# Performance work log

Measured on AMD Instinct MI355X. Metric: run time of the kernel, lower is better.

Reference implementation:

```python
import jax, jax.numpy as jnp
import numpy as np
from jax import lax


def setup_inputs() -> dict:
    key = jax.random.key(0)
    k1, k2 = jax.random.split(key)
    B, T, C, U, W = 8, 4096, 512, 512, 2
    inputs = jax.random.normal(k1, (B, T, C), dtype=jnp.float32)
    kernel = jax.random.normal(k2, (W, C, 3 * U), dtype=jnp.float32) * (1.0 / np.sqrt(W * C))
    bias = jnp.zeros((3 * U,), dtype=jnp.float32)
    return {"inputs": inputs, "kernel": kernel, "bias": bias}


def _fo_pool(x, f):
    # x, f: [B, T, U]; c_t = f_t * c_{t-1} + (1 - f_t) * x_t, c_0 = 0
    xT = jnp.swapaxes(x, 0, 1)  # [T, B, U]
    fT = jnp.swapaxes(f, 0, 1)
    c0 = jnp.zeros(x.shape[:1] + x.shape[2:], dtype=x.dtype)  # [B, U]

    def step(c, fx):
        ft, xt = fx
        c = ft * c + (1.0 - ft) * xt
        return c, c

    _, cT = lax.scan(step, c0, (fT, xT))
    return jnp.swapaxes(cT, 0, 1)  # [B, T, U]


def reference(inputs, kernel, bias):
    # Conv1D, padding='same', stride=1, NWC layout
    gates = lax.conv_general_dilated(
        inputs, kernel, window_strides=(1,), padding='SAME',
        dimension_numbers=('NWC', 'WIO', 'NWC')) + bias  # [B, T, 3U]
    x, forget, output = jnp.split(gates, 3, axis=-1)
    x = jnp.tanh(x)
    forget = jax.nn.sigmoid(forget)
    c = _fo_pool(x, forget)
    h = jax.nn.sigmoid(output) * c
    return h
```

## Files before the change

kernel.cpp:

```cpp
#include <hip/hip_runtime.h>

typedef unsigned short u16;
typedef unsigned int u32;
typedef _Float16 f16;
typedef __attribute__((ext_vector_type(8))) _Float16 half8;
typedef __attribute__((ext_vector_type(2))) __fp16 fp16x2;
typedef __attribute__((ext_vector_type(4))) float float4_;
typedef __attribute__((ext_vector_type(4))) unsigned short ushort4_;
typedef __attribute__((ext_vector_type(4))) unsigned int u32x4;

union hu { f16 h; u16 u; };

__device__ __forceinline__ u32 pkrtz(float a, float b) {
    fp16x2 t = __builtin_amdgcn_cvt_pkrtz(a, b);
    union { fp16x2 h; u32 u; } cv; cv.h = t;
    return cv.u;
}

__device__ __forceinline__ void gl16(const u16* g, u16* l) {
    __builtin_amdgcn_global_load_lds(
        (const __attribute__((address_space(1))) void*)g,
        (__attribute__((address_space(3))) void*)l, 16, 0, 0);
}

#define Bsz 8
#define Tsz 4096
#define Csz 512
#define Usz 512
#define NG  1536
#define KK  1024
#define MM  32768
#define NCH 128
#define CHL 32

__global__ void prep_a(const float* __restrict__ in, u16* __restrict__ A16) {
    int gid = blockIdx.x * 256 + threadIdx.x;
    int idx8 = gid * 8;
    int c8 = idx8 & 511;
    int row = idx8 >> 9;
    int b = (u32)row / 4097u;
    int t = row - b * 4097;
    u32x4 w;
    if (t == Tsz) {
        w = (u32x4)0;
    } else {
        const float* p = in + ((size_t)(b * Tsz + t) << 9) + c8;
        float4_ v0 = *(const float4_*)p;
        float4_ v1 = *(const float4_*)(p + 4);
        w.x = pkrtz(v0.x, v0.y); w.y = pkrtz(v0.z, v0.w);
        w.z = pkrtz(v1.x, v1.y); w.w = pkrtz(v1.z, v1.w);
    }
    *(u32x4*)(A16 + idx8) = w;
}

__global__ void prep_k(const float* __restrict__ kern, u16* __restrict__ KT) {
    __shared__ u16 t[64][70];
    const int k0 = blockIdx.x * 64;
    const int n0 = blockIdx.y * 64;
    const int tid = threadIdx.x;
    #pragma unroll
    for (int it = 0; it < 16; ++it) {
        int s = it * 256 + tid;
        int r = s >> 6;
        int c = s & 63;
        float v = kern[(size_t)(k0 + r) * NG + n0 + c];
        hu cv; cv.h = (f16)v;
        t[c][r] = cv.u;
    }
    __syncthreads();
    #pragma unroll
    for (int it = 0; it < 4; ++it) {
        int s = it * 256 + tid;
        int n = s >> 4;
        int kq = (s & 15) * 4;
        ushort4_ w;
        w.x = t[n][kq]; w.y = t[n][kq + 1]; w.z = t[n][kq + 2]; w.w = t[n][kq + 3];
        *(ushort4_*)(KT + (size_t)(n0 + n) * KK + k0 + kq) = w;
    }
}

#define LDS_A 8192
#define LDS_B 16384

__device__ __forceinline__ void stage_A(const u16* __restrict__ A16, u16* dst,
                                        int arow_base, int kin, int tid, int lane) {
    #pragma unroll
    for (int it = 0; it < 2; ++it) {
        int s = it * 512 + tid;
        int row = s >> 3, p = s & 7;
        int c = p ^ (row & 7);
        gl16(A16 + (((size_t)(arow_base + row)) << 9) + kin + c * 8, dst + (s - lane) * 8);
    }
}

__device__ __forceinline__ void stage_B_it(const u16* __restrict__ KT, u16* dst,
                                           int n0, int kc, int it, int tid, int lane) {
    int s = it * 512 + tid;
    int row = s >> 3, p = s & 7;
    int c = p ^ (row & 7);
    gl16(KT + (((size_t)(n0 + row)) << 10) + kc + c * 8, dst + (s - lane) * 8);
}

__global__ __launch_bounds__(512, 2) void gemm_gates(
    const u16* __restrict__ A16, const u16* __restrict__ KT,
    const float* __restrict__ bias,
    u16* __restrict__ X, u16* __restrict__ F, float* __restrict__ O)
{
    __shared__ u16 lA[3 * LDS_A];
    __shared__ u16 lB[3 * LDS_B];

    const int tid  = threadIdx.x;
    const int lane = tid & 63;
    const int wave = tid >> 6;

    const int orig = blockIdx.x;
    const int wg = (orig & 7) * 192 + (orig >> 3);
    const int nb = wg % 6;
    const int mb = wg / 6;
    const int m0 = mb * 128;
    const int n0 = nb * 256;
    const int b  = m0 >> 12;
    const int t0 = m0 & 4095;
    const int arow0 = b * (Tsz + 1) + t0;

    float4_ acc[4][4];
    #pragma unroll
    for (int i = 0; i < 4; ++i)
        #pragma unroll
        for (int j = 0; j < 4; ++j) acc[i][j] = (float4_)0.0f;

    const int wm = (wave >> 2) * 64;
    const int wn = (wave & 3) * 64;
    const int arow = wm + (lane & 15);
    const int brow = wn + (lane & 15);
    const int q   = lane >> 4;
    const int swz = lane & 7;

    stage_A(A16, lA, arow0, 0, tid, lane);
    #pragma unroll
    for (int it = 0; it < 4; ++it) stage_B_it(KT, lB, n0, 0, it, tid, lane);
    stage_A(A16, lA + LDS_A, arow0, 64, tid, lane);
    #pragma unroll
    for (int it = 0; it < 4; ++it) stage_B_it(KT, lB + LDS_B, n0, 64, it, tid, lane);

    int buf = 0;
    #pragma unroll 1
    for (int kt = 0; kt < 16; ++kt) {
        if (kt < 15) asm volatile("s_waitcnt vmcnt(6)" ::: "memory");
        else         asm volatile("s_waitcnt vmcnt(0)" ::: "memory");
        __builtin_amdgcn_s_barrier();

        const u16* a  = lA + buf * LDS_A;
        const u16* bs = lB + buf * LDS_B;
        const int nbuf = (buf >= 1) ? buf - 1 : 2;
        const int kt2 = kt + 2;
        const bool st = kt2 < 16;
        const int kc2 = kt2 * 64;

        half8 fa[4][2], fb01[2][2];
        #pragma unroll
        for (int mi = 0; mi < 4; ++mi)
            #pragma unroll
            for (int s2 = 0; s2 < 2; ++s2)
                fa[mi][s2] = *(const half8*)(a + (arow + mi * 16) * 64 + (((s2 * 4 + q) ^ swz) * 8));
        #pragma unroll
        for (int ni = 0; ni < 2; ++ni)
            #pragma unroll
            for (int s2 = 0; s2 < 2; ++s2)
                fb01[ni][s2] = *(const half8*)(bs + (brow + ni * 16) * 64 + (((s2 * 4 + q) ^ swz) * 8));
        if (st) {
            stage_A(A16, lA + nbuf * LDS_A, arow0 + (kt2 >> 3), (kt2 & 7) * 64, tid, lane);
            stage_B_it(KT, lB + nbuf * LDS_B, n0, kc2, 0, tid, lane);
        }
        __builtin_amdgcn_s_barrier();
        asm volatile("s_waitcnt lgkmcnt(0)" ::: "memory");
        __builtin_amdgcn_s_setprio(1);
        #pragma unroll
        for (int s2 = 0; s2 < 2; ++s2)
            #pragma unroll
            for (int mi = 0; mi < 4; ++mi)
                #pragma unroll
                for (int ni = 0; ni < 2; ++ni)
                    acc[mi][ni] = __builtin_amdgcn_mfma_f32_16x16x32_f16(fa[mi][s2], fb01[ni][s2], acc[mi][ni], 0, 0, 0);
        __builtin_amdgcn_s_setprio(0);
        __builtin_amdgcn_s_barrier();

        half8 fb23[2][2];
        #pragma unroll
        for (int ni = 0; ni < 2; ++ni)
            #pragma unroll
            for (int s2 = 0; s2 < 2; ++s2)
                fb23[ni][s2] = *(const half8*)(bs + (brow + 32 + ni * 16) * 64 + (((s2 * 4 + q) ^ swz) * 8));
        if (st) {
            stage_B_it(KT, lB + nbuf * LDS_B, n0, kc2, 1, tid, lane);
            stage_B_it(KT, lB + nbuf * LDS_B, n0, kc2, 2, tid, lane);
            stage_B_it(KT, lB + nbuf * LDS_B, n0, kc2, 3, tid, lane);
        }
        __builtin_amdgcn_s_barrier();
        asm volatile("s_waitcnt lgkmcnt(0)" ::: "memory");
        __builtin_amdgcn_s_setprio(1);
        #pragma unroll
        for (int s2 = 0; s2 < 2; ++s2)
            #pragma unroll
            for (int mi = 0; mi < 4; ++mi)
                #pragma unroll
                for (int ni = 0; ni < 2; ++ni)
                    acc[mi][ni + 2] = __builtin_amdgcn_mfma_f32_16x16x32_f16(fa[mi][s2], fb23[ni][s2], acc[mi][ni + 2], 0, 0, 0);
        __builtin_amdgcn_s_setprio(0);

        buf = (buf == 2) ? 0 : buf + 1;
    }

    const int plane = nb >> 1;
    const int rq = q * 4;
    const int cl = lane & 15;
    #pragma unroll
    for (int mi = 0; mi < 4; ++mi)
        #pragma unroll
        for (int ni = 0; ni < 4; ++ni) {
            const int gm = m0 + wm + mi * 16 + rq;
            const int gn = n0 + wn + ni * 16 + cl;
            const float bv = bias[gn];
            const int cp = gn & 511;
            #pragma unroll
            for (int r2 = 0; r2 < 4; ++r2) {
                float v = acc[mi][ni][r2] + bv;
                if (plane == 0) {
                    float res = 1.0f - 2.0f / (__expf(2.0f * v) + 1.0f);
                    hu cv; cv.h = (f16)res;
                    X[(size_t)(gm + r2) * Usz + cp] = cv.u;
                } else if (plane == 1) {
                    float res = 1.0f / (1.0f + __expf(-v));
                    hu cv; cv.h = (f16)res;
                    F[(size_t)(gm + r2) * Usz + cp] = cv.u;
                } else {
                    float res = 1.0f / (1.0f + __expf(-v));
                    O[(size_t)(gm + r2) * Usz + cp] = res;
                }
            }
        }
}

__device__ __forceinline__ float4_ x4(const u16* p) {
    ushort4_ xr = *(const ushort4_*)p;
    float4_ xv;
    #pragma unroll
    for (int j = 0; j < 4; ++j) { hu cv; cv.u = xr[j]; xv[j] = (float)cv.h; }
    return xv;
}

__global__ void scan_chunk(const u16* __restrict__ F, const u16* __restrict__ X,
                           float* __restrict__ CA, float* __restrict__ CB) {
    int g = blockIdx.x * 256 + threadIdx.x;
    int u4 = (g & 127) * 4;
    int bc = g >> 7;
    size_t base = (size_t)bc * CHL * Usz + u4;
    float4_ c = (float4_)0.0f, A = (float4_)1.0f;
    for (int i = 0; i < CHL; ++i) {
        float4_ fv = x4(F + base + (size_t)i * Usz);
        float4_ xv = x4(X + base + (size_t)i * Usz);
        c = fv * c + (1.0f - fv) * xv;
        A = A * fv;
    }
    *(float4_*)(CA + (size_t)bc * Usz + u4) = A;
    *(float4_*)(CB + (size_t)bc * Usz + u4) = c;
}

__global__ void scan_prefix(const float* __restrict__ CA, const float* __restrict__ CB,
                            float* __restrict__ CS) {
    int g = blockIdx.x * 256 + threadIdx.x;
    int u = g & 511;
    int b = g >> 9;
    float c = 0.0f;
    #pragma unroll 16
    for (int ch = 0; ch < NCH; ++ch) {
        int idx = (b * NCH + ch) * Usz + u;
        CS[idx] = c;
        c = CA[idx] * c + CB[idx];
    }
}

__global__ void scan_final(const u16* __restrict__ F, const u16* __restrict__ X,
                           const float* __restrict__ CS, float* __restrict__ out) {
    int g = blockIdx.x * 256 + threadIdx.x;
    int u4 = (g & 127) * 4;
    int bc = g >> 7;
    size_t base = (size_t)bc * CHL * Usz + u4;
    float4_ c = *(const float4_*)(CS + (size_t)bc * Usz + u4);
    for (int i = 0; i < CHL; ++i) {
        float4_ fv = x4(F + base + (size_t)i * Usz);
        float4_ xv = x4(X + base + (size_t)i * Usz);
        c = fv * c + (1.0f - fv) * xv;
        float4_ ov = *(const float4_*)(out + base + (size_t)i * Usz);
        *(float4_*)(out + base + (size_t)i * Usz) = ov * c;
    }
}

extern "C" void kernel_launch(void* const* d_in, const int* in_sizes, int n_in,
                              void* d_out, int out_size, void* d_ws, size_t ws_size,
                              hipStream_t stream) {
    const float* in   = (const float*)d_in[0];
    const float* kern = (const float*)d_in[1];
    const float* bias = (const float*)d_in[2];
    float* out = (float*)d_out;
    char* ws = (char*)d_ws;

    const size_t A16_B  = (size_t)Bsz * (Tsz + 1) * Csz * 2;
    const size_t OFF_KT = A16_B;
    const size_t OFF_F  = OFF_KT + (size_t)NG * KK * 2;
    const size_t OFF_X  = OFF_F + (size_t)MM * Usz * 2;
    const size_t NEED   = OFF_X + (size_t)MM * Usz * 2;

    if (ws_size < NEED) return;

    u16*   A16 = (u16*)ws;
    u16*   KT  = (u16*)(ws + OFF_KT);
    u16*   Fh  = (u16*)(ws + OFF_F);
    u16*   Xb  = (u16*)(ws + OFF_X);
    const size_t CH = (size_t)Bsz * NCH * Usz;
    float* CA = (float*)ws;
    float* CB = CA + CH;
    float* CS = CB + CH;

    prep_a<<<(int)(A16_B / 16 / 256), 256, 0, stream>>>(in, A16);
    prep_k<<<dim3(KK / 64, NG / 64), 256, 0, stream>>>(kern, KT);
    gemm_gates<<<(MM / 128) * (NG / 256), 512, 0, stream>>>(A16, KT, bias, Xb, Fh, out);
    scan_chunk<<<Bsz * NCH * Usz / 4 / 256, 256, 0, stream>>>(Fh, Xb, CA, CB);
    scan_prefix<<<Bsz * Usz / 256, 256, 0, stream>>>(CA, CB, CS);
    scan_final<<<Bsz * NCH * Usz / 4 / 256, 256, 0, stream>>>(Fh, Xb, CS, out);
}
```

Measured before the change: 317.0 us.

## Enlarge GEMM tile to 256x256 with K=32 stages and fewer barriers

The gates GEMM moves from a 128x256 block tile with 64-wide K stages to a 256x256 tile with 32-wide K stages. Each wave now owns a 128x64 sub-tile with 32 accumulators, reusing the B fragments across two A halves. The XOR LDS swizzle is dropped, and the mid-iteration barriers and explicit lgkmcnt waits are replaced by sched_barriers. The aim is more MFMA work per LDS byte and less synchronisation. In exchange the accumulator count doubles under a 512x2 launch bound, which risks register spills, the unswizzled LDS reads may hit bank conflicts, and the grid shrinks to 768 blocks, about 1.5 waves.

Result: faster. 302.0 us (-4.7%).

```diff
diff --git a/kernel.cpp b/kernel.cpp
--- a/kernel.cpp
+++ b/kernel.cpp
@@ -79,26 +79,26 @@
     }
 }
 
-#define LDS_A 8192
-#define LDS_B 16384
-
-__device__ __forceinline__ void stage_A(const u16* __restrict__ A16, u16* dst,
+#define LDS_T 8192
+
+__device__ __forceinline__ void stageA3(const u16* __restrict__ A16, u16* dst,
                                         int arow_base, int kin, int tid, int lane) {
     #pragma unroll
     for (int it = 0; it < 2; ++it) {
         int s = it * 512 + tid;
-        int row = s >> 3, p = s & 7;
-        int c = p ^ (row & 7);
+        int row = s >> 2, c = s & 3;
         gl16(A16 + (((size_t)(arow_base + row)) << 9) + kin + c * 8, dst + (s - lane) * 8);
     }
 }
 
-__device__ __forceinline__ void stage_B_it(const u16* __restrict__ KT, u16* dst,
-                                           int n0, int kc, int it, int tid, int lane) {
-    int s = it * 512 + tid;
-    int row = s >> 3, p = s & 7;
-    int c = p ^ (row & 7);
-    gl16(KT + (((size_t)(n0 + row)) << 10) + kc + c * 8, dst + (s - lane) * 8);
+__device__ __forceinline__ void stageB3(const u16* __restrict__ KT, u16* dst,
+                                        int n0, int kk, int tid, int lane) {
+    #pragma unroll
+    for (int it = 0; it < 2; ++it) {
+        int s = it * 512 + tid;
+        int row = s >> 2, c = s & 3;
+        gl16(KT + (((size_t)(n0 + row)) << 10) + kk + c * 8, dst + (s - lane) * 8);
+    }
 }
 
 __global__ __launch_bounds__(512, 2) void gemm_gates(
@@ -106,120 +106,95 @@
     const float* __restrict__ bias,
     u16* __restrict__ X, u16* __restrict__ F, float* __restrict__ O)
 {
-    __shared__ u16 lA[3 * LDS_A];
-    __shared__ u16 lB[3 * LDS_B];
+    __shared__ u16 lA[3 * LDS_T];
+    __shared__ u16 lB[3 * LDS_T];
 
     const int tid  = threadIdx.x;
     const int lane = tid & 63;
     const int wave = tid >> 6;
 
     const int orig = blockIdx.x;
-    const int wg = (orig & 7) * 192 + (orig >> 3);
+    const int wg = (orig & 7) * 96 + (orig >> 3);
     const int nb = wg % 6;
     const int mb = wg / 6;
-    const int m0 = mb * 128;
+    const int m0 = mb * 256;
     const int n0 = nb * 256;
     const int b  = m0 >> 12;
     const int t0 = m0 & 4095;
     const int arow0 = b * (Tsz + 1) + t0;
 
-    float4_ acc[4][4];
-    #pragma unroll
-    for (int i = 0; i < 4; ++i)
+    float4_ acc[8][4];
+    #pragma unroll
+    for (int i = 0; i < 8; ++i)
         #pragma unroll
         for (int j = 0; j < 4; ++j) acc[i][j] = (float4_)0.0f;
 
-    const int wm = (wave >> 2) * 64;
+    const int wm = (wave >> 2) * 128;
     const int wn = (wave & 3) * 64;
-    const int arow = wm + (lane & 15);
-    const int brow = wn + (lane & 15);
-    const int q   = lane >> 4;
-    const int swz = lane & 7;
-
-    stage_A(A16, lA, arow0, 0, tid, lane);
-    #pragma unroll
-    for (int it = 0; it < 4; ++it) stage_B_it(KT, lB, n0, 0, it, tid, lane);
-    stage_A(A16, lA + LDS_A, arow0, 64, tid, lane);
-    #pragma unroll
-    for (int it = 0; it < 4; ++it) stage_B_it(KT, lB + LDS_B, n0, 64, it, tid, lane);
+    const int fr = lane & 15;
+    const int fq = lane >> 4;
+
+    stageA3(A16, lA, arow0, 0, tid, lane);
+    stageB3(KT, lB, n0, 0, tid, lane);
+    stageA3(A16, lA + LDS_T, arow0, 32, tid, lane);
+    stageB3(KT, lB + LDS_T, n0, 32, tid, lane);
 
     int buf = 0;
     #pragma unroll 1
-    for (int kt = 0; kt < 16; ++kt) {
-        if (kt < 15) asm volatile("s_waitcnt vmcnt(6)" ::: "memory");
+    for (int kt = 0; kt < 32; ++kt) {
+        if (kt < 31) asm volatile("s_waitcnt vmcnt(4)" ::: "memory");
         else         asm volatile("s_waitcnt vmcnt(0)" ::: "memory");
         __builtin_amdgcn_s_barrier();
 
-        const u16* a  = lA + buf * LDS_A;
-        const u16* bs = lB + buf * LDS_B;
+        const u16* a  = lA + buf * LDS_T;
+        const u16* bs = lB + buf * LDS_T;
         const int nbuf = (buf >= 1) ? buf - 1 : 2;
         const int kt2 = kt + 2;
-        const bool st = kt2 < 16;
-        const int kc2 = kt2 * 64;
-
-        half8 fa[4][2], fb01[2][2];
+        const int kk2 = kt2 * 32;
+        const bool st = kt2 < 32;
+
+        half8 fa[4], fb[4];
+        #pragma unroll
+        for (int j = 0; j < 4; ++j)
+            fa[j] = *(const half8*)(a + (wm + j * 16 + fr) * 32 + fq * 8);
+        #pragma unroll
+        for (int n = 0; n < 4; ++n)
+            fb[n] = *(const half8*)(bs + (wn + n * 16 + fr) * 32 + fq * 8);
+        if (st) stageA3(A16, lA + nbuf * LDS_T, arow0 + (kk2 >> 9), kk2 & 511, tid, lane);
+        __builtin_amdgcn_sched_barrier(0);
+        __builtin_amdgcn_s_setprio(1);
         #pragma unroll
         for (int mi = 0; mi < 4; ++mi)
             #pragma unroll
-            for (int s2 = 0; s2 < 2; ++s2)
-                fa[mi][s2] = *(const half8*)(a + (arow + mi * 16) * 64 + (((s2 * 4 + q) ^ swz) * 8));
-        #pragma unroll
-        for (int ni = 0; ni < 2; ++ni)
+            for (int ni = 0; ni < 4; ++ni)
+                acc[mi][ni] = __builtin_amdgcn_mfma_f32_16x16x32_f16(fa[mi], fb[ni], acc[mi][ni], 0, 0, 0);
+        __builtin_amdgcn_s_setprio(0);
+
+        half8 fa2[4];
+        #pragma unroll
+        for (int j = 0; j < 4; ++j)
+            fa2[j] = *(const half8*)(a + (wm + 64 + j * 16 + fr) * 32 + fq * 8);
+        if (st) stageB3(KT, lB + nbuf * LDS_T, n0, kk2, tid, lane);
+        __builtin_amdgcn_sched_barrier(0);
+        __builtin_amdgcn_s_setprio(1);
+        #pragma unroll
+        for (int mi = 0; mi < 4; ++mi)
             #pragma unroll
-            for (int s2 = 0; s2 < 2; ++s2)
-                fb01[ni][s2] = *(const half8*)(bs + (brow + ni * 16) * 64 + (((s2 * 4 + q) ^ swz) * 8));
-        if (st) {
-            stage_A(A16, lA + nbuf * LDS_A, arow0 + (kt2 >> 3), (kt2 & 7) * 64, tid, lane);
-            stage_B_it(KT, lB + nbuf * LDS_B, n0, kc2, 0, tid, lane);
-        }
-        __builtin_amdgcn_s_barrier();
-        asm volatile("s_waitcnt lgkmcnt(0)" ::: "memory");
-        __builtin_amdgcn_s_setprio(1);
-        #pragma unroll
-        for (int s2 = 0; s2 < 2; ++s2)
-            #pragma unroll
-            for (int mi = 0; mi < 4; ++mi)
-                #pragma unroll
-                for (int ni = 0; ni < 2; ++ni)
-                    acc[mi][ni] = __builtin_amdgcn_mfma_f32_16x16x32_f16(fa[mi][s2], fb01[ni][s2], acc[mi][ni], 0, 0, 0);
+            for (int ni = 0; ni < 4; ++ni)
+                acc[4 + mi][ni] = __builtin_amdgcn_mfma_f32_16x16x32_f16(fa2[mi], fb[ni], acc[4 + mi][ni], 0, 0, 0);
         __builtin_amdgcn_s_setprio(0);
-        __builtin_amdgcn_s_barrier();
-
-        half8 fb23[2][2];
-        #pragma unroll
-        for (int ni = 0; ni < 2; ++ni)
-            #pragma unroll
-            for (int s2 = 0; s2 < 2; ++s2)
-                fb23[ni][s2] = *(const half8*)(bs + (brow + 32 + ni * 16) * 64 + (((s2 * 4 + q) ^ swz) * 8));
-        if (st) {
-            stage_B_it(KT, lB + nbuf * LDS_B, n0, kc2, 1, tid, lane);
-            stage_B_it(KT, lB + nbuf * LDS_B, n0, kc2, 2, tid, lane);
-            stage_B_it(KT, lB + nbuf * LDS_B, n0, kc2, 3, tid, lane);
-        }
-        __builtin_amdgcn_s_barrier();
-        asm volatile("s_waitcnt lgkmcnt(0)" ::: "memory");
-        __builtin_amdgcn_s_setprio(1);
-        #pragma unroll
-        for (int s2 = 0; s2 < 2; ++s2)
-            #pragma unroll
-            for (int mi = 0; mi < 4; ++mi)
-                #pragma unroll
-                for (int ni = 0; ni < 2; ++ni)
-                    acc[mi][ni + 2] = __builtin_amdgcn_mfma_f32_16x16x32_f16(fa[mi][s2], fb23[ni][s2], acc[mi][ni + 2], 0, 0, 0);
-        __builtin_amdgcn_s_setprio(0);
 
         buf = (buf == 2) ? 0 : buf + 1;
     }
 
     const int plane = nb >> 1;
-    const int rq = q * 4;
-    const int cl = lane & 15;
-    #pragma unroll
-    for (int mi = 0; mi < 4; ++mi)
+    const int rq = fq * 4;
+    #pragma unroll
+    for (int mi = 0; mi < 8; ++mi)
         #pragma unroll
         for (int ni = 0; ni < 4; ++ni) {
             const int gm = m0 + wm + mi * 16 + rq;
-            const int gn = n0 + wn + ni * 16 + cl;
+            const int gn = n0 + wn + ni * 16 + fr;
             const float bv = bias[gn];
             const int cp = gn & 511;
             #pragma unroll
@@ -324,7 +299,7 @@
 
     prep_a<<<(int)(A16_B / 16 / 256), 256, 0, stream>>>(in, A16);
     prep_k<<<dim3(KK / 64, NG / 64), 256, 0, stream>>>(kern, KT);
-    gemm_gates<<<(MM / 128) * (NG / 256), 512, 0, stream>>>(A16, KT, bias, Xb, Fh, out);
+    gemm_gates<<<(MM / 256) * (NG / 256), 512, 0, stream>>>(A16, KT, bias, Xb, Fh, out);
     scan_chunk<<<Bsz * NCH * Usz / 4 / 256, 256, 0, stream>>>(Fh, Xb, CA, CB);
     scan_prefix<<<Bsz * Usz / 256, 256, 0, stream>>>(CA, CB, CS);
     scan_final<<<Bsz * NCH * Usz / 4 / 256, 256, 0, stream>>>(Fh, Xb, CS, out);
```
